# Kernel optimization log

Measured on AMD Instinct MI355X. Metric: run time of the kernel, lower is better.

Reference implementation:

```python
import jax, jax.numpy as jnp
import numpy as np

B, N, C = 4, 4096, 2048
EPS = 1e-5  # torch.nn.LayerNorm default


def setup_inputs() -> dict:
    key = jax.random.key(0)
    kx, = jax.random.split(key, 1)
    x = jax.random.normal(kx, (B, N, C), dtype=jnp.float32)
    gamma = jnp.ones((C,), dtype=jnp.float32)   # LayerNorm weight
    beta = jnp.zeros((C,), dtype=jnp.float32)   # LayerNorm bias
    return {"x": x, "gamma": gamma, "beta": beta}


def reference(x, gamma, beta):
    # The original repeats x to (B,N,N,C), applies a (no-op on the diagonal)
    # triu mask, FFTs every row over C, and extracts the (n,n) diagonal.
    # The diagonal rows are exactly the unmasked originals, so this equals:
    #   LayerNorm(real(fft(x, axis=-1)))
    y = jnp.fft.fft(x, axis=-1).real  # (B,N,C)
    mu = jnp.mean(y, axis=-1, keepdims=True)
    var = jnp.mean(jnp.square(y - mu), axis=-1, keepdims=True)  # biased, as torch LN
    return (y - mu) * jax.lax.rsqrt(var + EPS) * gamma + beta
```

## Files before the change

### kernel.cpp

```cpp
#include <hip/hip_runtime.h>
#include <math.h>


#define TPB 256
#define CD  2048
#define PAD(j) ((j) + ((j) >> 3))

__device__ __forceinline__ float2 f2add(float2 a, float2 b) { return make_float2(a.x + b.x, a.y + b.y); }
__device__ __forceinline__ float2 f2sub(float2 a, float2 b) { return make_float2(a.x - b.x, a.y - b.y); }
__device__ __forceinline__ float2 cmul(float2 a, float2 b) {
    return make_float2(a.x * b.x - a.y * b.y, a.x * b.y + a.y * b.x);
}

template<int S_>
__device__ __forceinline__ void r8_store(float2* buf, int t, const float2* x)
{
    float2 a0 = f2add(x[0], x[4]), a1 = f2add(x[1], x[5]);
    float2 a2 = f2add(x[2], x[6]), a3 = f2add(x[3], x[7]);
    float2 b0 = f2sub(x[0], x[4]), b1 = f2sub(x[1], x[5]);
    float2 b2 = f2sub(x[2], x[6]), b3 = f2sub(x[3], x[7]);
    float2 c0 = f2add(a0, a2), c1 = f2sub(a0, a2);
    float2 d0 = f2add(a1, a3), d1 = f2sub(a1, a3);
    float2 X0 = f2add(c0, d0), X4 = f2sub(c0, d0);
    float2 X2 = make_float2(c1.x + d1.y, c1.y - d1.x);
    float2 X6 = make_float2(c1.x - d1.y, c1.y + d1.x);
    const float R2 = 0.70710678118654752440f;
    float2 y1 = make_float2((b1.x + b1.y) * R2, (b1.y - b1.x) * R2);
    float2 y2 = make_float2(b2.y, -b2.x);
    float2 y3 = make_float2((b3.y - b3.x) * R2, -(b3.x + b3.y) * R2);
    float2 e0 = f2add(b0, y2), e1p = f2sub(b0, y2);
    float2 f0 = f2add(y1, y3), f1 = f2sub(y1, y3);
    float2 X1 = f2add(e0, f0), X5 = f2sub(e0, f0);
    float2 X3 = make_float2(e1p.x + f1.y, e1p.y - f1.x);
    float2 X7 = make_float2(e1p.x - f1.y, e1p.y + f1.x);

    const int q = t & (S_ - 1);
    const int p = t / S_;
    const float th = -6.28318530717958647692f * (float)S_ / 2048.0f;
    float sw, cw;
    __sincosf(th * (float)p, &sw, &cw);
    const float2 e1 = make_float2(cw, sw);
    const int o = q + 8 * S_ * p;
    buf[PAD(o)] = X0;
    float2 cur = e1;
    buf[PAD(o + 1 * S_)] = cmul(X1, cur); cur = cmul(cur, e1);
    buf[PAD(o + 2 * S_)] = cmul(X2, cur); cur = cmul(cur, e1);
    buf[PAD(o + 3 * S_)] = cmul(X3, cur); cur = cmul(cur, e1);
    buf[PAD(o + 4 * S_)] = cmul(X4, cur); cur = cmul(cur, e1);
    buf[PAD(o + 5 * S_)] = cmul(X5, cur); cur = cmul(cur, e1);
    buf[PAD(o + 6 * S_)] = cmul(X6, cur); cur = cmul(cur, e1);
    buf[PAD(o + 7 * S_)] = cmul(X7, cur);
}

__global__ __launch_bounds__(TPB, 8) void fourier_ln_kernel(
    const float* __restrict__ x,
    const float* __restrict__ gamma,
    const float* __restrict__ beta,
    float* __restrict__ out)
{
    __shared__ float2 buf[2304];
    __shared__ float red[16];
    __shared__ float bc[4];

    const int t = threadIdx.x;
    const long long row0 = 2LL * (long long)blockIdx.x;
    const long long row1 = row0 + 1;
    const float* xr = x + row0 * CD;
    const float* xi = x + row1 * CD;

    {
        float2 v[8];
#pragma unroll
        for (int k = 0; k < 8; k++)
            v[k] = make_float2(xr[t + 256 * k], xi[t + 256 * k]);
        r8_store<1>(buf, t, v);
    }
    __syncthreads();

    {
        float2 v[8];
#pragma unroll
        for (int k = 0; k < 8; k++) v[k] = buf[PAD(t + 256 * k)];
        __syncthreads();
        r8_store<8>(buf, t, v);
    }
    __syncthreads();

    {
        float2 v[8];
#pragma unroll
        for (int k = 0; k < 8; k++) v[k] = buf[PAD(t + 256 * k)];
        __syncthreads();
        r8_store<64>(buf, t, v);
    }
    __syncthreads();

    {
        float2 w[8];
#pragma unroll
        for (int h = 0; h < 2; h++)
#pragma unroll
            for (int k = 0; k < 4; k++)
                w[4 * h + k] = buf[PAD(t + 256 * h + 512 * k)];
        __syncthreads();
#pragma unroll
        for (int h = 0; h < 2; h++) {
            float2 c0 = f2add(w[4 * h + 0], w[4 * h + 2]);
            float2 c1 = f2sub(w[4 * h + 0], w[4 * h + 2]);
            float2 d0 = f2add(w[4 * h + 1], w[4 * h + 3]);
            float2 d1 = f2sub(w[4 * h + 1], w[4 * h + 3]);
            const int b = t + 256 * h;
            buf[PAD(b)]        = f2add(c0, d0);
            buf[PAD(b + 512)]  = make_float2(c1.x + d1.y, c1.y - d1.x);
            buf[PAD(b + 1024)] = f2sub(c0, d0);
            buf[PAD(b + 1536)] = make_float2(c1.x - d1.y, c1.y + d1.x);
        }
    }
    __syncthreads();

    float y0v[8], y1v[8];
    float s0 = 0.f, ss0 = 0.f, s1 = 0.f, ss1 = 0.f;
#pragma unroll
    for (int jj = 0; jj < 2; jj++) {
#pragma unroll
        for (int c = 0; c < 4; c++) {
            int k = 4 * t + c + 1024 * jj;
            float2 zk = buf[PAD(k)];
            float2 zr = buf[PAD((CD - k) & (CD - 1))];
            float a = 0.5f * (zk.x + zr.x);
            float b = 0.5f * (zk.y + zr.y);
            y0v[4 * jj + c] = a; y1v[4 * jj + c] = b;
            s0 += a; ss0 += a * a;
            s1 += b; ss1 += b * b;
        }
    }

#pragma unroll
    for (int off = 32; off > 0; off >>= 1) {
        s0  += __shfl_down(s0,  off, 64);
        ss0 += __shfl_down(ss0, off, 64);
        s1  += __shfl_down(s1,  off, 64);
        ss1 += __shfl_down(ss1, off, 64);
    }
    const int wave = t >> 6;
    if ((t & 63) == 0) {
        red[4 * wave + 0] = s0;
        red[4 * wave + 1] = ss0;
        red[4 * wave + 2] = s1;
        red[4 * wave + 3] = ss1;
    }
    __syncthreads();
    if (t == 0) {
        float S0 = 0.f, SS0 = 0.f, S1 = 0.f, SS1 = 0.f;
#pragma unroll
        for (int w = 0; w < 4; w++) {
            S0 += red[4 * w + 0]; SS0 += red[4 * w + 1];
            S1 += red[4 * w + 2]; SS1 += red[4 * w + 3];
        }
        const float inv = 1.0f / (float)CD;
        float mu0 = S0 * inv, mu1 = S1 * inv;
        float v0 = SS0 * inv - mu0 * mu0;
        float v1 = SS1 * inv - mu1 * mu1;
        bc[0] = mu0; bc[1] = rsqrtf(v0 + 1e-5f);
        bc[2] = mu1; bc[3] = rsqrtf(v1 + 1e-5f);
    }
    __syncthreads();
    const float mu0 = bc[0], r0 = bc[1];
    const float mu1 = bc[2], r1 = bc[3];

    const float4* g4 = (const float4*)gamma;
    const float4* b4 = (const float4*)beta;
    float4* o0 = (float4*)(out + row0 * CD);
    float4* o1 = (float4*)(out + row1 * CD);
#pragma unroll
    for (int jj = 0; jj < 2; jj++) {
        int idx = t + 256 * jj;
        float4 g = g4[idx];
        float4 be = b4[idx];
        float4 r0v, r1v;
        r0v.x = (y0v[4 * jj + 0] - mu0) * r0 * g.x + be.x;
        r0v.y = (y0v[4 * jj + 1] - mu0) * r0 * g.y + be.y;
        r0v.z = (y0v[4 * jj + 2] - mu0) * r0 * g.z + be.z;
        r0v.w = (y0v[4 * jj + 3] - mu0) * r0 * g.w + be.w;
        r1v.x = (y1v[4 * jj + 0] - mu1) * r1 * g.x + be.x;
        r1v.y = (y1v[4 * jj + 1] - mu1) * r1 * g.y + be.y;
        r1v.z = (y1v[4 * jj + 2] - mu1) * r1 * g.z + be.z;
        r1v.w = (y1v[4 * jj + 3] - mu1) * r1 * g.w + be.w;
        o0[idx] = r0v;
        o1[idx] = r1v;
    }
}

extern "C" void kernel_launch(void* const* d_in, const int* in_sizes, int n_in,
                              void* d_out, int out_size, void* d_ws, size_t ws_size,
                              hipStream_t stream) {
    (void)in_sizes; (void)n_in; (void)d_ws; (void)ws_size; (void)out_size;
    const float* x     = (const float*)d_in[0];
    const float* gamma = (const float*)d_in[1];
    const float* beta  = (const float*)d_in[2];
    float* out = (float*)d_out;

    const int total_rows = 4 * 4096;
    const int blocks = total_rows / 2;
    fourier_ln_kernel<<<blocks, TPB, 0, stream>>>(x, gamma, beta, out);
}
```

Baseline: 232.6 us.

## Make blocks persistent over row pairs with register prefetch of next input

The grid shrinks to 2048 blocks, and each block now loops over four row pairs. During each iteration it loads the next pair's input into registers, so global load latency overlaps with the FFT and LayerNorm work on the current pair. This cuts block launch overhead and hides memory latency. The cost is extra registers, and launch bounds drop from 8 to 6 blocks per CU, which lowers occupancy.

Measured after the change: 468.7 us. +101.5%, slower.

```diff
diff --git a/kernel.cpp b/kernel.cpp
--- a/kernel.cpp
+++ b/kernel.cpp
@@ -2,8 +2,10 @@
 #include <math.h>
 
 
-#define TPB 256
-#define CD  2048
+#define TPB  256
+#define CD   2048
+#define NBLK 2048
+#define PPB  4
 #define PAD(j) ((j) + ((j) >> 3))
 
 __device__ __forceinline__ float2 f2add(float2 a, float2 b) { return make_float2(a.x + b.x, a.y + b.y); }
@@ -52,7 +54,7 @@
     buf[PAD(o + 7 * S_)] = cmul(X7, cur);
 }
 
-__global__ __launch_bounds__(TPB, 8) void fourier_ln_kernel(
+__global__ __launch_bounds__(TPB, 6) void fourier_ln_kernel(
     const float* __restrict__ x,
     const float* __restrict__ gamma,
     const float* __restrict__ beta,
@@ -63,131 +65,160 @@
     __shared__ float bc[4];
 
     const int t = threadIdx.x;
-    const long long row0 = 2LL * (long long)blockIdx.x;
-    const long long row1 = row0 + 1;
-    const float* xr = x + row0 * CD;
-    const float* xi = x + row1 * CD;
-
+
+    float xr_c[8], xi_c[8];
     {
-        float2 v[8];
-#pragma unroll
-        for (int k = 0; k < 8; k++)
-            v[k] = make_float2(xr[t + 256 * k], xi[t + 256 * k]);
-        r8_store<1>(buf, t, v);
+        const float* xr = x + (size_t)(2 * blockIdx.x) * CD;
+        const float* xi = xr + CD;
+#pragma unroll
+        for (int k = 0; k < 8; k++) {
+            xr_c[k] = xr[t + 256 * k];
+            xi_c[k] = xi[t + 256 * k];
+        }
     }
-    __syncthreads();
-
-    {
-        float2 v[8];
-#pragma unroll
-        for (int k = 0; k < 8; k++) v[k] = buf[PAD(t + 256 * k)];
-        __syncthreads();
-        r8_store<8>(buf, t, v);
-    }
-    __syncthreads();
-
-    {
-        float2 v[8];
-#pragma unroll
-        for (int k = 0; k < 8; k++) v[k] = buf[PAD(t + 256 * k)];
-        __syncthreads();
-        r8_store<64>(buf, t, v);
-    }
-    __syncthreads();
-
-    {
-        float2 w[8];
-#pragma unroll
-        for (int h = 0; h < 2; h++)
-#pragma unroll
-            for (int k = 0; k < 4; k++)
-                w[4 * h + k] = buf[PAD(t + 256 * h + 512 * k)];
-        __syncthreads();
-#pragma unroll
-        for (int h = 0; h < 2; h++) {
-            float2 c0 = f2add(w[4 * h + 0], w[4 * h + 2]);
-            float2 c1 = f2sub(w[4 * h + 0], w[4 * h + 2]);
-            float2 d0 = f2add(w[4 * h + 1], w[4 * h + 3]);
-            float2 d1 = f2sub(w[4 * h + 1], w[4 * h + 3]);
-            const int b = t + 256 * h;
-            buf[PAD(b)]        = f2add(c0, d0);
-            buf[PAD(b + 512)]  = make_float2(c1.x + d1.y, c1.y - d1.x);
-            buf[PAD(b + 1024)] = f2sub(c0, d0);
-            buf[PAD(b + 1536)] = make_float2(c1.x - d1.y, c1.y + d1.x);
-        }
-    }
-    __syncthreads();
-
-    float y0v[8], y1v[8];
-    float s0 = 0.f, ss0 = 0.f, s1 = 0.f, ss1 = 0.f;
-#pragma unroll
-    for (int jj = 0; jj < 2; jj++) {
-#pragma unroll
-        for (int c = 0; c < 4; c++) {
-            int k = 4 * t + c + 1024 * jj;
-            float2 zk = buf[PAD(k)];
-            float2 zr = buf[PAD((CD - k) & (CD - 1))];
-            float a = 0.5f * (zk.x + zr.x);
-            float b = 0.5f * (zk.y + zr.y);
-            y0v[4 * jj + c] = a; y1v[4 * jj + c] = b;
-            s0 += a; ss0 += a * a;
-            s1 += b; ss1 += b * b;
-        }
-    }
-
-#pragma unroll
-    for (int off = 32; off > 0; off >>= 1) {
-        s0  += __shfl_down(s0,  off, 64);
-        ss0 += __shfl_down(ss0, off, 64);
-        s1  += __shfl_down(s1,  off, 64);
-        ss1 += __shfl_down(ss1, off, 64);
-    }
-    const int wave = t >> 6;
-    if ((t & 63) == 0) {
-        red[4 * wave + 0] = s0;
-        red[4 * wave + 1] = ss0;
-        red[4 * wave + 2] = s1;
-        red[4 * wave + 3] = ss1;
-    }
-    __syncthreads();
-    if (t == 0) {
-        float S0 = 0.f, SS0 = 0.f, S1 = 0.f, SS1 = 0.f;
-#pragma unroll
-        for (int w = 0; w < 4; w++) {
-            S0 += red[4 * w + 0]; SS0 += red[4 * w + 1];
-            S1 += red[4 * w + 2]; SS1 += red[4 * w + 3];
-        }
-        const float inv = 1.0f / (float)CD;
-        float mu0 = S0 * inv, mu1 = S1 * inv;
-        float v0 = SS0 * inv - mu0 * mu0;
-        float v1 = SS1 * inv - mu1 * mu1;
-        bc[0] = mu0; bc[1] = rsqrtf(v0 + 1e-5f);
-        bc[2] = mu1; bc[3] = rsqrtf(v1 + 1e-5f);
-    }
-    __syncthreads();
-    const float mu0 = bc[0], r0 = bc[1];
-    const float mu1 = bc[2], r1 = bc[3];
-
-    const float4* g4 = (const float4*)gamma;
-    const float4* b4 = (const float4*)beta;
-    float4* o0 = (float4*)(out + row0 * CD);
-    float4* o1 = (float4*)(out + row1 * CD);
-#pragma unroll
-    for (int jj = 0; jj < 2; jj++) {
-        int idx = t + 256 * jj;
-        float4 g = g4[idx];
-        float4 be = b4[idx];
-        float4 r0v, r1v;
-        r0v.x = (y0v[4 * jj + 0] - mu0) * r0 * g.x + be.x;
-        r0v.y = (y0v[4 * jj + 1] - mu0) * r0 * g.y + be.y;
-        r0v.z = (y0v[4 * jj + 2] - mu0) * r0 * g.z + be.z;
-        r0v.w = (y0v[4 * jj + 3] - mu0) * r0 * g.w + be.w;
-        r1v.x = (y1v[4 * jj + 0] - mu1) * r1 * g.x + be.x;
-        r1v.y = (y1v[4 * jj + 1] - mu1) * r1 * g.y + be.y;
-        r1v.z = (y1v[4 * jj + 2] - mu1) * r1 * g.z + be.z;
-        r1v.w = (y1v[4 * jj + 3] - mu1) * r1 * g.w + be.w;
-        o0[idx] = r0v;
-        o1[idx] = r1v;
+
+    for (int j = 0; j < PPB; ++j) {
+        const int pair = blockIdx.x + j * NBLK;
+
+        float xr_n[8], xi_n[8];
+        if (j + 1 < PPB) {
+            const float* xr = x + (size_t)(2 * (pair + NBLK)) * CD;
+            const float* xi = xr + CD;
+#pragma unroll
+            for (int k = 0; k < 8; k++) {
+                xr_n[k] = xr[t + 256 * k];
+                xi_n[k] = xi[t + 256 * k];
+            }
+        }
+
+        {
+            float2 v[8];
+#pragma unroll
+            for (int k = 0; k < 8; k++) v[k] = make_float2(xr_c[k], xi_c[k]);
+            r8_store<1>(buf, t, v);
+        }
+        __syncthreads();
+
+        {
+            float2 v[8];
+#pragma unroll
+            for (int k = 0; k < 8; k++) v[k] = buf[PAD(t + 256 * k)];
+            __syncthreads();
+            r8_store<8>(buf, t, v);
+        }
+        __syncthreads();
+
+        {
+            float2 v[8];
+#pragma unroll
+            for (int k = 0; k < 8; k++) v[k] = buf[PAD(t + 256 * k)];
+            __syncthreads();
+            r8_store<64>(buf, t, v);
+        }
+        __syncthreads();
+
+        {
+            float2 w[8];
+#pragma unroll
+            for (int h = 0; h < 2; h++)
+#pragma unroll
+                for (int k = 0; k < 4; k++)
+                    w[4 * h + k] = buf[PAD(t + 256 * h + 512 * k)];
+            __syncthreads();
+#pragma unroll
+            for (int h = 0; h < 2; h++) {
+                float2 c0 = f2add(w[4 * h + 0], w[4 * h + 2]);
+                float2 c1 = f2sub(w[4 * h + 0], w[4 * h + 2]);
+                float2 d0 = f2add(w[4 * h + 1], w[4 * h + 3]);
+                float2 d1 = f2sub(w[4 * h + 1], w[4 * h + 3]);
+                const int b = t + 256 * h;
+                buf[PAD(b)]        = f2add(c0, d0);
+                buf[PAD(b + 512)]  = make_float2(c1.x + d1.y, c1.y - d1.x);
+                buf[PAD(b + 1024)] = f2sub(c0, d0);
+                buf[PAD(b + 1536)] = make_float2(c1.x - d1.y, c1.y + d1.x);
+            }
+        }
+        __syncthreads();
+
+        float y0v[8], y1v[8];
+        float s0 = 0.f, ss0 = 0.f, s1 = 0.f, ss1 = 0.f;
+#pragma unroll
+        for (int jj = 0; jj < 2; jj++) {
+#pragma unroll
+            for (int c = 0; c < 4; c++) {
+                int k = 4 * t + c + 1024 * jj;
+                float2 zk = buf[PAD(k)];
+                float2 zr = buf[PAD((CD - k) & (CD - 1))];
+                float a = 0.5f * (zk.x + zr.x);
+                float b = 0.5f * (zk.y + zr.y);
+                y0v[4 * jj + c] = a; y1v[4 * jj + c] = b;
+                s0 += a; ss0 += a * a;
+                s1 += b; ss1 += b * b;
+            }
+        }
+
+#pragma unroll
+        for (int off = 32; off > 0; off >>= 1) {
+            s0  += __shfl_down(s0,  off, 64);
+            ss0 += __shfl_down(ss0, off, 64);
+            s1  += __shfl_down(s1,  off, 64);
+            ss1 += __shfl_down(ss1, off, 64);
+        }
+        const int wave = t >> 6;
+        if ((t & 63) == 0) {
+            red[4 * wave + 0] = s0;
+            red[4 * wave + 1] = ss0;
+            red[4 * wave + 2] = s1;
+            red[4 * wave + 3] = ss1;
+        }
+        __syncthreads();
+        if (t == 0) {
+            float S0 = 0.f, SS0 = 0.f, S1 = 0.f, SS1 = 0.f;
+#pragma unroll
+            for (int w = 0; w < 4; w++) {
+                S0 += red[4 * w + 0]; SS0 += red[4 * w + 1];
+                S1 += red[4 * w + 2]; SS1 += red[4 * w + 3];
+            }
+            const float inv = 1.0f / (float)CD;
+            float mu0 = S0 * inv, mu1 = S1 * inv;
+            float v0 = SS0 * inv - mu0 * mu0;
+            float v1 = SS1 * inv - mu1 * mu1;
+            bc[0] = mu0; bc[1] = rsqrtf(v0 + 1e-5f);
+            bc[2] = mu1; bc[3] = rsqrtf(v1 + 1e-5f);
+        }
+        __syncthreads();
+        const float mu0 = bc[0], r0 = bc[1];
+        const float mu1 = bc[2], r1 = bc[3];
+
+        const float4* g4 = (const float4*)gamma;
+        const float4* b4 = (const float4*)beta;
+        float4* o0 = (float4*)(out + (size_t)(2 * pair) * CD);
+        float4* o1 = (float4*)(out + (size_t)(2 * pair + 1) * CD);
+#pragma unroll
+        for (int jj = 0; jj < 2; jj++) {
+            int idx = t + 256 * jj;
+            float4 g = g4[idx];
+            float4 be = b4[idx];
+            float4 r0v, r1v;
+            r0v.x = (y0v[4 * jj + 0] - mu0) * r0 * g.x + be.x;
+            r0v.y = (y0v[4 * jj + 1] - mu0) * r0 * g.y + be.y;
+            r0v.z = (y0v[4 * jj + 2] - mu0) * r0 * g.z + be.z;
+            r0v.w = (y0v[4 * jj + 3] - mu0) * r0 * g.w + be.w;
+            r1v.x = (y1v[4 * jj + 0] - mu1) * r1 * g.x + be.x;
+            r1v.y = (y1v[4 * jj + 1] - mu1) * r1 * g.y + be.y;
+            r1v.z = (y1v[4 * jj + 2] - mu1) * r1 * g.z + be.z;
+            r1v.w = (y1v[4 * jj + 3] - mu1) * r1 * g.w + be.w;
+            o0[idx] = r0v;
+            o1[idx] = r1v;
+        }
+
+        if (j + 1 < PPB) {
+#pragma unroll
+            for (int k = 0; k < 8; k++) {
+                xr_c[k] = xr_n[k];
+                xi_c[k] = xi_n[k];
+            }
+        }
     }
 }
 
@@ -200,7 +231,5 @@
     const float* beta  = (const float*)d_in[2];
     float* out = (float*)d_out;
 
-    const int total_rows = 4 * 4096;
-    const int blocks = total_rows / 2;
-    fourier_ln_kernel<<<blocks, TPB, 0, stream>>>(x, gamma, beta, out);
-}
+    fourier_ln_kernel<<<NBLK, TPB, 0, stream>>>(x, gamma, beta, out);
+}
```
